# Optimization experiments

Hardware: AMD Instinct MI355X
Metric: run time of the kernel (lower is better)

Reference implementation:

```python
import jax, jax.numpy as jnp
import numpy as np

EMSIZE = 1024
NHEAD = 16
HEAD = EMSIZE // NHEAD


def setup_inputs() -> dict:
    key = jax.random.key(0)
    ks = jax.random.split(key, 8)
    s = 1.0 / np.sqrt(EMSIZE)
    return {
        "embed": jax.random.normal(ks[0], (2, 2048, EMSIZE), dtype=jnp.float32),
        "q": jax.random.normal(ks[1], (2, 2048, EMSIZE), dtype=jnp.float32),
        "Wk": jax.random.normal(ks[2], (EMSIZE, EMSIZE), dtype=jnp.float32) * s,
        "bk": jnp.zeros((EMSIZE,), dtype=jnp.float32),
        "Wq": jax.random.normal(ks[3], (EMSIZE, EMSIZE), dtype=jnp.float32) * s,
        "bq": jnp.zeros((EMSIZE,), dtype=jnp.float32),
        "Wv": jax.random.normal(ks[4], (EMSIZE, EMSIZE), dtype=jnp.float32) * s,
        "bv": jnp.zeros((EMSIZE,), dtype=jnp.float32),
    }


def _split_heads(x):
    # [b, s, E] -> [b, h, s, d]
    b, s, _ = x.shape
    return x.reshape(b, s, NHEAD, HEAD).transpose(0, 2, 1, 3)


def reference(embed, q, Wk, bk, Wq, bq, Wv, bv):
    # torch Linear: y = x @ W.T + b
    k = _split_heads(embed @ Wk.T + bk)   # [b, h, skv, d]
    qh = _split_heads(q @ Wq.T + bq)      # [b, h, sq, d]
    v = _split_heads(embed @ Wv.T + bv)   # [b, h, skv, d]
    scale = 1.0 / np.sqrt(HEAD).astype(np.float32)
    scores = jnp.einsum("bhqd,bhkd->bhqk", qh, k) * scale
    attn = jax.nn.softmax(scores, axis=-1)  # dropout p=0 -> identity
    ctx = jnp.einsum("bhqk,bhkd->bhqd", attn, v)
    b, h, sq, d = ctx.shape
    return ctx.transpose(0, 2, 1, 3).reshape(b, sq, h * d)
```

## Files before the change

### kernel.cpp

```cpp
#include <hip/hip_runtime.h>
#include <cstdint>
#include <cstddef>


using bf16 = __bf16;
typedef __bf16 bf16x8 __attribute__((ext_vector_type(8)));
typedef float f32x4 __attribute__((ext_vector_type(4)));
typedef float f32x16 __attribute__((ext_vector_type(16)));
using uint32 = unsigned int;

__device__ __forceinline__ void async16(void* lds, const void* g) {
  __builtin_amdgcn_global_load_lds((__attribute__((address_space(1))) void*)g,
                                   (__attribute__((address_space(3))) void*)lds,
                                   16, 0, 0);
}

__device__ __forceinline__ uint32 pack_bf16x2(float lo, float hi_) {
  union { bf16 h[2]; uint32 u; } w;
  w.h[0] = (bf16)lo; w.h[1] = (bf16)hi_;
  return w.u;
}

__global__ void cast_all_kernel(const float* __restrict__ e, const float* __restrict__ q,
                                const float* __restrict__ wk, const float* __restrict__ wq,
                                const float* __restrict__ wv, bf16* __restrict__ dst) {
  int i = blockIdx.x * blockDim.x + threadIdx.x;
  if (i >= 2883584) return;
  const float* src; int off;
  if (i < 1048576)      { src = e;  off = 0; }
  else if (i < 2097152) { src = q;  off = 1048576; }
  else if (i < 2359296) { src = wk; off = 2097152; }
  else if (i < 2621440) { src = wq; off = 2359296; }
  else                  { src = wv; off = 2621440; }
  float4 v = reinterpret_cast<const float4*>(src)[i - off];
  union { bf16 h[4]; unsigned long long u; } o;
  o.h[0] = (bf16)v.x; o.h[1] = (bf16)v.y; o.h[2] = (bf16)v.z; o.h[3] = (bf16)v.w;
  reinterpret_cast<unsigned long long*>(dst)[i] = o.u;
}

__global__ __launch_bounds__(256) void proj_kernel(
    const bf16* __restrict__ emb, const bf16* __restrict__ qin,
    const bf16* __restrict__ wk, const bf16* __restrict__ wq, const bf16* __restrict__ wv,
    const float* __restrict__ bk, const float* __restrict__ bq, const float* __restrict__ bv,
    bf16* __restrict__ Kp, bf16* __restrict__ Qp, bf16* __restrict__ Vt)
{
  __shared__ bf16 As[128 * 64];
  __shared__ bf16 Bs[128 * 64];

  int bid = blockIdx.x;
  int xcd = bid & 7;
  int k_ = bid >> 3;
  int p = xcd * 12 + (k_ >> 3);
  int n = k_ & 7;
  int proj = p >> 5;
  int m0 = (p & 31) * 128;
  int n0 = n * 128;

  const bf16* A = (proj == 1) ? qin : emb;
  const bf16* W = (proj == 0) ? wk : (proj == 1) ? wq : wv;
  const float* bias = (proj == 0) ? bk : (proj == 1) ? bq : bv;
  const bool proj2 = (proj == 2);

  int tid = threadIdx.x;
  int lane = tid & 63, wid = tid >> 6;
  int quad = lane >> 4, l16 = lane & 15;
  int moff = (wid & 1) * 64, noff = (wid >> 1) * 64;

  f32x4 zero = {0.f, 0.f, 0.f, 0.f};
  f32x4 acc[4][4];
#pragma unroll
  for (int i = 0; i < 4; i++)
#pragma unroll
    for (int j = 0; j < 4; j++) acc[i][j] = zero;

  for (int kk = 0; kk < 1024; kk += 64) {
    __syncthreads();
#pragma unroll
    for (int i = 0; i < 4; i++) {
      int c = i * 256 + tid;
      int row = c >> 3;
      int ko = ((c ^ row) & 7) << 3;
      async16(&As[(size_t)(i * 256 + wid * 64) * 8], &A[(size_t)(m0 + row) * 1024 + kk + ko]);
      async16(&Bs[(size_t)(i * 256 + wid * 64) * 8], &W[(size_t)(n0 + row) * 1024 + kk + ko]);
    }
    __syncthreads();
#pragma unroll
    for (int ks = 0; ks < 2; ks++) {
      bf16x8 af[4], bfr[4];
#pragma unroll
      for (int i = 0; i < 4; i++) {
        int row = moff + i * 16 + l16;
        af[i] = *reinterpret_cast<const bf16x8*>(&As[row * 64 + ((((ks << 2) | quad) ^ row) & 7) * 8]);
      }
#pragma unroll
      for (int j = 0; j < 4; j++) {
        int row = noff + j * 16 + l16;
        bfr[j] = *reinterpret_cast<const bf16x8*>(&Bs[row * 64 + ((((ks << 2) | quad) ^ row) & 7) * 8]);
      }
      if (proj2) {
#pragma unroll
        for (int i = 0; i < 4; i++)
#pragma unroll
          for (int j = 0; j < 4; j++)
            acc[i][j] = __builtin_amdgcn_mfma_f32_16x16x32_bf16(bfr[j], af[i], acc[i][j], 0, 0, 0);
      } else {
#pragma unroll
        for (int i = 0; i < 4; i++)
#pragma unroll
          for (int j = 0; j < 4; j++)
            acc[i][j] = __builtin_amdgcn_mfma_f32_16x16x32_bf16(af[i], bfr[j], acc[i][j], 0, 0, 0);
      }
    }
  }

  if (proj2) {
#pragma unroll
    for (int i = 0; i < 4; i++) {
      int grow = m0 + moff + i * 16 + l16;
      int bb = grow >> 11;
      int ss = grow & 2047;
#pragma unroll
      for (int j = 0; j < 4; j++) {
#pragma unroll
        for (int r = 0; r < 4; r++) {
          int gcol = n0 + noff + j * 16 + quad * 4 + r;
          int hh = gcol >> 6, dd = gcol & 63;
          int bh = bb * 16 + hh;
          float v = acc[i][j][r] + bias[gcol];
          Vt[((size_t)bh * 64 + dd) * 2048 + ss] = (bf16)v;
        }
      }
    }
  } else {
    float bvv[4];
#pragma unroll
    for (int j = 0; j < 4; j++) bvv[j] = bias[n0 + noff + j * 16 + l16];
    bf16* dst = (proj == 0) ? Kp : Qp;
    const float qs = (proj == 1) ? 0.18033688011112042f : 1.0f;
#pragma unroll
    for (int i = 0; i < 4; i++) {
#pragma unroll
      for (int r = 0; r < 4; r++) {
        int grow = m0 + moff + i * 16 + quad * 4 + r;
        int bb = grow >> 11;
        int ss = grow & 2047;
#pragma unroll
        for (int j = 0; j < 4; j++) {
          int gcol = n0 + noff + j * 16 + l16;
          int hh = gcol >> 6, dd = gcol & 63;
          int bh = bb * 16 + hh;
          float v = (acc[i][j][r] + bvv[j]) * qs;
          dst[((size_t)bh * 2048 + ss) * 64 + dd] = (bf16)v;
        }
      }
    }
  }
}

__global__ __launch_bounds__(512, 4) void attn_kernel(
    const bf16* __restrict__ Qp, const bf16* __restrict__ Kp, const bf16* __restrict__ Vt,
    float* __restrict__ out)
{
  __shared__ bf16 Ks[2][64 * 64];
  __shared__ bf16 Vs[2][64 * 64];
  __shared__ float lshare[256];

  int swz = (blockIdx.x & 7) * 64 + (blockIdx.x >> 3);
  int qblk = swz & 15;
  int bh = swz >> 4;
  int q0 = qblk << 7;
  int bb = bh >> 4, hh = bh & 15;

  const bf16* Qg = Qp + (size_t)bh * (2048 * 64);
  const bf16* Kg = Kp + (size_t)bh * (2048 * 64);
  const bf16* Vg = Vt + (size_t)bh * (64 * 2048);

  int tid = threadIdx.x, lane = tid & 63, wid = tid >> 6;
  int l32 = lane & 31;
  int h = lane >> 5;
  int qw = wid & 3;
  int t = wid >> 2;
  int wq0 = q0 + qw * 32;

  auto stage = [&](int kt_, int buf) {
    int c = tid;
    int row = c >> 3;
    int srow = (row & ~12) | ((row & 4) << 1) | ((row & 8) >> 1);
    int ko = ((c ^ row) & 7) << 3;
    async16(&Ks[buf][(size_t)(wid * 64) * 8], &Kg[(size_t)(kt_ * 64 + srow) * 64 + ko]);
    async16(&Vs[buf][(size_t)(wid * 64) * 8], &Vg[(size_t)row * 2048 + kt_ * 64 + ko]);
  };

  bf16x8 qf[4];
#pragma unroll
  for (int s = 0; s < 4; s++)
    qf[s] = *reinterpret_cast<const bf16x8*>(
        &Qg[(size_t)(wq0 + l32) * 64 + s * 16 + h * 8]);

  stage(0, 0);

  const f32x16 z16 = {0.f, 0.f, 0.f, 0.f, 0.f, 0.f, 0.f, 0.f,
                      0.f, 0.f, 0.f, 0.f, 0.f, 0.f, 0.f, 0.f};
  f32x16 Ov[2];
  Ov[0] = z16; Ov[1] = z16;
  float2 l2;
  l2.x = 0.f; l2.y = 0.f;

  int row = t * 32 + l32;

  for (int kt = 0; kt < 32; kt++) {
    int cur = kt & 1;
    __syncthreads();
    __builtin_amdgcn_sched_barrier(0);
    if (kt < 31) stage(kt + 1, cur ^ 1);
    __builtin_amdgcn_sched_barrier(0);

    const bf16* Kc = Ks[cur];
    const bf16* Vc = Vs[cur];

    f32x16 St;
    {
      bf16x8 kf = *reinterpret_cast<const bf16x8*>(&Kc[row * 64 + ((h ^ row) & 7) * 8]);
      St = __builtin_amdgcn_mfma_f32_32x32x16_bf16(kf, qf[0], z16, 0, 0, 0);
    }
#pragma unroll
    for (int s = 1; s < 4; s++) {
      int j8 = s * 2 + h;
      bf16x8 kf = *reinterpret_cast<const bf16x8*>(&Kc[row * 64 + ((j8 ^ row) & 7) * 8]);
      St = __builtin_amdgcn_mfma_f32_32x32x16_bf16(kf, qf[s], St, 0, 0, 0);
    }

    uint32 pk[8];
#pragma unroll
    for (int i = 0; i < 8; i++) {
      float pe = __builtin_amdgcn_exp2f(St[2 * i]);
      float po = __builtin_amdgcn_exp2f(St[2 * i + 1]);
      l2.x += pe; l2.y += po;
      pk[i] = pack_bf16x2(pe, po);
    }

#pragma unroll
    for (int g = 0; g < 2; g++) {
      union { uint32 u[4]; bf16x8 v; } pb;
#pragma unroll
      for (int i = 0; i < 4; i++) pb.u[i] = pk[g * 4 + i];
      int j8 = t * 4 + g * 2 + h;
#pragma unroll
      for (int dt = 0; dt < 2; dt++) {
        int rowv = dt * 32 + l32;
        bf16x8 vf = *reinterpret_cast<const bf16x8*>(&Vc[rowv * 64 + ((j8 ^ rowv) & 7) * 8]);
        Ov[dt] = __builtin_amdgcn_mfma_f32_32x32x16_bf16(vf, pb.v, Ov[dt], 0, 0, 0);
      }
    }
  }

  __syncthreads();
  float* c0 = reinterpret_cast<float*>(&Ks[0][0]);
  float* c1 = reinterpret_cast<float*>(&Vs[0][0]);
  float lh = l2.x + l2.y;
  if (t == 1) {
#pragma unroll
    for (int g = 0; g < 4; g++) {
      int ci = (g * 256 + qw * 64 + lane) * 4;
      float4 a, b;
      a.x = Ov[0][4 * g + 0]; a.y = Ov[0][4 * g + 1];
      a.z = Ov[0][4 * g + 2]; a.w = Ov[0][4 * g + 3];
      b.x = Ov[1][4 * g + 0]; b.y = Ov[1][4 * g + 1];
      b.z = Ov[1][4 * g + 2]; b.w = Ov[1][4 * g + 3];
      *reinterpret_cast<float4*>(&c0[ci]) = a;
      *reinterpret_cast<float4*>(&c1[ci]) = b;
    }
    lshare[qw * 64 + lane] = lh;
  }
  __syncthreads();
  if (t == 0) {
#pragma unroll
    for (int g = 0; g < 4; g++) {
      int ci = (g * 256 + qw * 64 + lane) * 4;
      float4 a = *reinterpret_cast<const float4*>(&c0[ci]);
      float4 b = *reinterpret_cast<const float4*>(&c1[ci]);
      Ov[0][4 * g + 0] += a.x; Ov[0][4 * g + 1] += a.y;
      Ov[0][4 * g + 2] += a.z; Ov[0][4 * g + 3] += a.w;
      Ov[1][4 * g + 0] += b.x; Ov[1][4 * g + 1] += b.y;
      Ov[1][4 * g + 2] += b.z; Ov[1][4 * g + 3] += b.w;
    }
    lh += lshare[qw * 64 + lane];
    float l_tot = lh + __shfl_xor(lh, 32);
    float inv = 1.0f / l_tot;
    int q = wq0 + l32;
    float* dstO = out + ((size_t)bb * 2048 + q) * 1024 + hh * 64;
#pragma unroll
    for (int dt = 0; dt < 2; dt++)
#pragma unroll
      for (int g = 0; g < 4; g++) {
        float4 o;
        o.x = Ov[dt][4 * g + 0] * inv;
        o.y = Ov[dt][4 * g + 1] * inv;
        o.z = Ov[dt][4 * g + 2] * inv;
        o.w = Ov[dt][4 * g + 3] * inv;
        *reinterpret_cast<float4*>(&dstO[dt * 32 + g * 8 + 4 * h]) = o;
      }
  }
}

extern "C" void kernel_launch(void* const* d_in, const int* in_sizes, int n_in,
                              void* d_out, int out_size, void* d_ws, size_t ws_size,
                              hipStream_t stream) {
  (void)in_sizes; (void)n_in; (void)out_size; (void)ws_size;
  const float* embed = (const float*)d_in[0];
  const float* qin   = (const float*)d_in[1];
  const float* Wk    = (const float*)d_in[2];
  const float* bk    = (const float*)d_in[3];
  const float* Wq    = (const float*)d_in[4];
  const float* bq    = (const float*)d_in[5];
  const float* Wv    = (const float*)d_in[6];
  const float* bv    = (const float*)d_in[7];
  float* out = (float*)d_out;

  bf16* ws = (bf16*)d_ws;
  bf16* emb_bf = ws;
  bf16* q_bf   = emb_bf + 4194304;
  bf16* wk_bf  = q_bf   + 4194304;
  bf16* wq_bf  = wk_bf  + 1048576;
  bf16* wv_bf  = wq_bf  + 1048576;
  bf16* Kp     = wv_bf  + 1048576;
  bf16* Qp     = Kp     + 4194304;
  bf16* Vt     = Qp     + 4194304;

  cast_all_kernel<<<11264, 256, 0, stream>>>(embed, qin, Wk, Wq, Wv, ws);

  proj_kernel<<<768, 256, 0, stream>>>(emb_bf, q_bf, wk_bf, wq_bf, wv_bf,
                                       bk, bq, bv, Kp, Qp, Vt);
  attn_kernel<<<512, 512, 0, stream>>>(Qp, Kp, Vt, out);
}
```

Before: 181.1 us.

## Load K/V fragments directly from global memory instead of staging through LDS

Removes the double-buffered async global-to-LDS staging of K and V tiles and instead has each lane load its MFMA operand fragments directly from global memory every iteration. The cross-wave __syncthreads is replaced by a plain s_barrier, and the shared arrays are re-declared only for the final reduction. This avoids the LDS round trip and ds_read traffic, but gives up shared reuse between waves (the four q-waves now each fetch the same K/V from cache) and loses the prefetch overlap, exposing global load latency inside the loop.

```diff
diff --git a/kernel.cpp b/kernel.cpp
--- a/kernel.cpp
+++ b/kernel.cpp
@@ -161,8 +161,8 @@
     const bf16* __restrict__ Qp, const bf16* __restrict__ Kp, const bf16* __restrict__ Vt,
     float* __restrict__ out)
 {
-  __shared__ bf16 Ks[2][64 * 64];
-  __shared__ bf16 Vs[2][64 * 64];
+  __shared__ float c0[4096];
+  __shared__ float c1[4096];
   __shared__ float lshare[256];
 
   int swz = (blockIdx.x & 7) * 64 + (blockIdx.x >> 3);
@@ -182,22 +182,17 @@
   int t = wid >> 2;
   int wq0 = q0 + qw * 32;
 
-  auto stage = [&](int kt_, int buf) {
-    int c = tid;
-    int row = c >> 3;
-    int srow = (row & ~12) | ((row & 4) << 1) | ((row & 8) >> 1);
-    int ko = ((c ^ row) & 7) << 3;
-    async16(&Ks[buf][(size_t)(wid * 64) * 8], &Kg[(size_t)(kt_ * 64 + srow) * 64 + ko]);
-    async16(&Vs[buf][(size_t)(wid * 64) * 8], &Vg[(size_t)row * 2048 + kt_ * 64 + ko]);
-  };
-
   bf16x8 qf[4];
 #pragma unroll
   for (int s = 0; s < 4; s++)
     qf[s] = *reinterpret_cast<const bf16x8*>(
         &Qg[(size_t)(wq0 + l32) * 64 + s * 16 + h * 8]);
 
-  stage(0, 0);
+  int r0 = t * 32 + l32;
+  int srow = (r0 & ~12) | ((r0 & 4) << 1) | ((r0 & 8) >> 1);
+  const bf16* Kl = Kg + (size_t)srow * 64 + h * 8;
+  const bf16* Vl0 = Vg + (size_t)l32 * 2048 + t * 32 + h * 8;
+  const bf16* Vl1 = Vl0 + (size_t)32 * 2048;
 
   const f32x16 z16 = {0.f, 0.f, 0.f, 0.f, 0.f, 0.f, 0.f, 0.f,
                       0.f, 0.f, 0.f, 0.f, 0.f, 0.f, 0.f, 0.f};
@@ -206,29 +201,26 @@
   float2 l2;
   l2.x = 0.f; l2.y = 0.f;
 
-  int row = t * 32 + l32;
-
   for (int kt = 0; kt < 32; kt++) {
-    int cur = kt & 1;
-    __syncthreads();
-    __builtin_amdgcn_sched_barrier(0);
-    if (kt < 31) stage(kt + 1, cur ^ 1);
-    __builtin_amdgcn_sched_barrier(0);
-
-    const bf16* Kc = Ks[cur];
-    const bf16* Vc = Vs[cur];
+    __builtin_amdgcn_s_barrier();
+
+    bf16x8 kf[4];
+#pragma unroll
+    for (int s = 0; s < 4; s++)
+      kf[s] = *reinterpret_cast<const bf16x8*>(&Kl[(size_t)kt * 4096 + s * 16]);
+
+    bf16x8 vf[2][2];
+#pragma unroll
+    for (int g = 0; g < 2; g++) {
+      vf[g][0] = *reinterpret_cast<const bf16x8*>(&Vl0[kt * 64 + g * 16]);
+      vf[g][1] = *reinterpret_cast<const bf16x8*>(&Vl1[kt * 64 + g * 16]);
+    }
 
     f32x16 St;
-    {
-      bf16x8 kf = *reinterpret_cast<const bf16x8*>(&Kc[row * 64 + ((h ^ row) & 7) * 8]);
-      St = __builtin_amdgcn_mfma_f32_32x32x16_bf16(kf, qf[0], z16, 0, 0, 0);
-    }
-#pragma unroll
-    for (int s = 1; s < 4; s++) {
-      int j8 = s * 2 + h;
-      bf16x8 kf = *reinterpret_cast<const bf16x8*>(&Kc[row * 64 + ((j8 ^ row) & 7) * 8]);
-      St = __builtin_amdgcn_mfma_f32_32x32x16_bf16(kf, qf[s], St, 0, 0, 0);
-    }
+    St = __builtin_amdgcn_mfma_f32_32x32x16_bf16(kf[0], qf[0], z16, 0, 0, 0);
+#pragma unroll
+    for (int s = 1; s < 4; s++)
+      St = __builtin_amdgcn_mfma_f32_32x32x16_bf16(kf[s], qf[s], St, 0, 0, 0);
 
     uint32 pk[8];
 #pragma unroll
@@ -244,19 +236,12 @@
       union { uint32 u[4]; bf16x8 v; } pb;
 #pragma unroll
       for (int i = 0; i < 4; i++) pb.u[i] = pk[g * 4 + i];
-      int j8 = t * 4 + g * 2 + h;
-#pragma unroll
-      for (int dt = 0; dt < 2; dt++) {
-        int rowv = dt * 32 + l32;
-        bf16x8 vf = *reinterpret_cast<const bf16x8*>(&Vc[rowv * 64 + ((j8 ^ rowv) & 7) * 8]);
-        Ov[dt] = __builtin_amdgcn_mfma_f32_32x32x16_bf16(vf, pb.v, Ov[dt], 0, 0, 0);
-      }
+      Ov[0] = __builtin_amdgcn_mfma_f32_32x32x16_bf16(vf[g][0], pb.v, Ov[0], 0, 0, 0);
+      Ov[1] = __builtin_amdgcn_mfma_f32_32x32x16_bf16(vf[g][1], pb.v, Ov[1], 0, 0, 0);
     }
   }
 
   __syncthreads();
-  float* c0 = reinterpret_cast<float*>(&Ks[0][0]);
-  float* c1 = reinterpret_cast<float*>(&Vs[0][0]);
   float lh = l2.x + l2.y;
   if (t == 1) {
 #pragma unroll
```

Result: slower. 256.5 us (+41.6%).

## Fuse activation fp32-to-bf16 cast into projection GEMM A-tile loads

Applied to the files above, without the earlier changes.

The separate cast of the embed and q activations to bf16 is removed. The projection kernel now loads fp32 A tiles into registers, converts and packs them to bf16, and writes them to LDS with a register prefetch of the next tile, while weights stay on the async global-to-LDS path. This avoids writing and re-reading 16M bf16 activation elements through global memory. In exchange, each projection block reads fp32 activations, twice the bytes, and eight column blocks re-read the same A rows. The A loads also become synchronous register loads, which adds VGPR pressure.

```diff
diff --git a/kernel.cpp b/kernel.cpp
--- a/kernel.cpp
+++ b/kernel.cpp
@@ -21,17 +21,14 @@
   return w.u;
 }
 
-__global__ void cast_all_kernel(const float* __restrict__ e, const float* __restrict__ q,
-                                const float* __restrict__ wk, const float* __restrict__ wq,
-                                const float* __restrict__ wv, bf16* __restrict__ dst) {
+__global__ void cast_w_kernel(const float* __restrict__ wk, const float* __restrict__ wq,
+                              const float* __restrict__ wv, bf16* __restrict__ dst) {
   int i = blockIdx.x * blockDim.x + threadIdx.x;
-  if (i >= 2883584) return;
+  if (i >= 786432) return;
   const float* src; int off;
-  if (i < 1048576)      { src = e;  off = 0; }
-  else if (i < 2097152) { src = q;  off = 1048576; }
-  else if (i < 2359296) { src = wk; off = 2097152; }
-  else if (i < 2621440) { src = wq; off = 2359296; }
-  else                  { src = wv; off = 2621440; }
+  if (i < 262144)      { src = wk; off = 0; }
+  else if (i < 524288) { src = wq; off = 262144; }
+  else                 { src = wv; off = 524288; }
   float4 v = reinterpret_cast<const float4*>(src)[i - off];
   union { bf16 h[4]; unsigned long long u; } o;
   o.h[0] = (bf16)v.x; o.h[1] = (bf16)v.y; o.h[2] = (bf16)v.z; o.h[3] = (bf16)v.w;
@@ -39,7 +36,7 @@
 }
 
 __global__ __launch_bounds__(256) void proj_kernel(
-    const bf16* __restrict__ emb, const bf16* __restrict__ qin,
+    const float* __restrict__ embf, const float* __restrict__ qinf,
     const bf16* __restrict__ wk, const bf16* __restrict__ wq, const bf16* __restrict__ wv,
     const float* __restrict__ bk, const float* __restrict__ bq, const float* __restrict__ bv,
     bf16* __restrict__ Kp, bf16* __restrict__ Qp, bf16* __restrict__ Vt)
@@ -56,7 +53,7 @@
   int m0 = (p & 31) * 128;
   int n0 = n * 128;
 
-  const bf16* A = (proj == 1) ? qin : emb;
+  const float* A = (proj == 1) ? qinf : embf;
   const bf16* W = (proj == 0) ? wk : (proj == 1) ? wq : wv;
   const float* bias = (proj == 0) ? bk : (proj == 1) ? bq : bv;
   const bool proj2 = (proj == 2);
@@ -66,24 +63,49 @@
   int quad = lane >> 4, l16 = lane & 15;
   int moff = (wid & 1) * 64, noff = (wid >> 1) * 64;
 
-  f32x4 zero = {0.f, 0.f, 0.f, 0.f};
-  f32x4 acc[4][4];
-#pragma unroll
-  for (int i = 0; i < 4; i++)
-#pragma unroll
-    for (int j = 0; j < 4; j++) acc[i][j] = zero;
-
-  for (int kk = 0; kk < 1024; kk += 64) {
-    __syncthreads();
+  float4 a0[4], a1[4];
+  auto loadA = [&](int it) {
 #pragma unroll
     for (int i = 0; i < 4; i++) {
       int c = i * 256 + tid;
       int row = c >> 3;
       int ko = ((c ^ row) & 7) << 3;
-      async16(&As[(size_t)(i * 256 + wid * 64) * 8], &A[(size_t)(m0 + row) * 1024 + kk + ko]);
-      async16(&Bs[(size_t)(i * 256 + wid * 64) * 8], &W[(size_t)(n0 + row) * 1024 + kk + ko]);
-    }
+      const float* src = &A[(size_t)(m0 + row) * 1024 + it * 64 + ko];
+      a0[i] = *reinterpret_cast<const float4*>(src);
+      a1[i] = *reinterpret_cast<const float4*>(src + 4);
+    }
+  };
+
+  f32x4 zero = {0.f, 0.f, 0.f, 0.f};
+  f32x4 acc[4][4];
+#pragma unroll
+  for (int i = 0; i < 4; i++)
+#pragma unroll
+    for (int j = 0; j < 4; j++) acc[i][j] = zero;
+
+  loadA(0);
+
+  for (int it = 0; it < 16; it++) {
     __syncthreads();
+#pragma unroll
+    for (int i = 0; i < 4; i++) {
+      union { uint32 u[4]; bf16x8 v; } pb;
+      pb.u[0] = pack_bf16x2(a0[i].x, a0[i].y);
+      pb.u[1] = pack_bf16x2(a0[i].z, a0[i].w);
+      pb.u[2] = pack_bf16x2(a1[i].x, a1[i].y);
+      pb.u[3] = pack_bf16x2(a1[i].z, a1[i].w);
+      *reinterpret_cast<bf16x8*>(&As[(size_t)(i * 256 + tid) * 8]) = pb.v;
+    }
+#pragma unroll
+    for (int i = 0; i < 4; i++) {
+      int c = i * 256 + tid;
+      int row = c >> 3;
+      int ko = ((c ^ row) & 7) << 3;
+      async16(&Bs[(size_t)(i * 256 + wid * 64) * 8], &W[(size_t)(n0 + row) * 1024 + it * 64 + ko]);
+    }
+    __syncthreads();
+    if (it < 15) loadA(it + 1);
+
 #pragma unroll
     for (int ks = 0; ks < 2; ks++) {
       bf16x8 af[4], bfr[4];
@@ -318,18 +340,16 @@
   float* out = (float*)d_out;
 
   bf16* ws = (bf16*)d_ws;
-  bf16* emb_bf = ws;
-  bf16* q_bf   = emb_bf + 4194304;
-  bf16* wk_bf  = q_bf   + 4194304;
+  bf16* wk_bf  = ws;
   bf16* wq_bf  = wk_bf  + 1048576;
   bf16* wv_bf  = wq_bf  + 1048576;
   bf16* Kp     = wv_bf  + 1048576;
   bf16* Qp     = Kp     + 4194304;
   bf16* Vt     = Qp     + 4194304;
 
-  cast_all_kernel<<<11264, 256, 0, stream>>>(embed, qin, Wk, Wq, Wv, ws);
-
-  proj_kernel<<<768, 256, 0, stream>>>(emb_bf, q_bf, wk_bf, wq_bf, wv_bf,
+  cast_w_kernel<<<3072, 256, 0, stream>>>(Wk, Wq, Wv, ws);
+
+  proj_kernel<<<768, 256, 0, stream>>>(embed, qin, wk_bf, wq_bf, wv_bf,
                                        bk, bq, bv, Kp, Qp, Vt);
   attn_kernel<<<512, 512, 0, stream>>>(Qp, Kp, Vt, out);
 }
```

New measurement: 212.9 us. 1.18x slower.
